# Optimization experiments

Hardware: AMD Instinct MI355X
Metric: run time of the kernel (lower is better)

## Reference

```python
import jax, jax.numpy as jnp
import numpy as np

DIM = 768


def setup_inputs() -> dict:
    key = jax.random.key(0)
    k1, k2, k3, k4, k5 = jax.random.split(key, 5)
    lines = jax.random.normal(k1, (32, 512, DIM), dtype=jnp.float32)
    videos = jax.random.normal(k2, (32, 128, DIM), dtype=jnp.float32)
    video_mask = jax.random.randint(k3, (32, 128), 0, 2, dtype=jnp.int32)
    # nn.Linear(dim, dim, bias=False) weights, applied as x @ W.T
    w_q = jax.random.normal(k4, (DIM, DIM), dtype=jnp.float32) * (DIM ** -0.5)
    w_k = jax.random.normal(k5, (DIM, DIM), dtype=jnp.float32) * (DIM ** -0.5)
    return {"lines": lines, "videos": videos, "video_mask": video_mask, "w_q": w_q, "w_k": w_k}


def reference(lines, videos, video_mask, w_q, w_k):
    scale = DIM ** -0.5
    q = jnp.einsum('bld,ed->ble', lines, w_q)   # (B, L, D)
    k = jnp.einsum('bvd,ed->bve', videos, w_k)  # (B, V, D)
    scores = jnp.einsum('bld,bvd->blv', q, k) * scale
    pad = (video_mask == 0)[:, None, :]          # (B, 1, V)
    scores = jnp.where(pad, jnp.float32(-1e9), scores)
    weights = jax.nn.softmax(scores, axis=-1)    # (B, L, V)
    return jnp.einsum('blv,bvd->bld', weights, videos)
```

## Files before the change

kernel.cpp:

```cpp
#include <hip/hip_runtime.h>

#define DIM 768
#define NB  32
#define LQ  512
#define NV  128

typedef unsigned short u16;
typedef unsigned int   u32;
typedef __bf16 bf16x8 __attribute__((ext_vector_type(8)));
typedef float  f32x4  __attribute__((ext_vector_type(4)));
typedef u16    u16x8  __attribute__((ext_vector_type(8)));
typedef u16    u16x4  __attribute__((ext_vector_type(4)));

typedef __attribute__((address_space(1))) const void gvoid;
typedef __attribute__((address_space(3))) void       svoid;

__device__ __forceinline__ u16 f2bf(float f) {
    u32 u = __float_as_uint(f);
    return (u16)((u + 0x7FFFu + ((u >> 16) & 1u)) >> 16);
}

__device__ __forceinline__ bf16x8 ld_frag(const u16* p) {
    return __builtin_bit_cast(bf16x8, *(const u16x8*)p);
}

__device__ __forceinline__ void gld16(const void* g, void* l) {
    __builtin_amdgcn_global_load_lds((gvoid*)g, (svoid*)l, 16, 0, 0);
}

__global__ __launch_bounds__(256) void cvt_kernel(const float* __restrict__ src,
                                                  u16* __restrict__ dst) {
    size_t i = (size_t)blockIdx.x * 256 + threadIdx.x;
    float4 a = ((const float4*)src)[i * 2];
    float4 b = ((const float4*)src)[i * 2 + 1];
    u16x8 o = { f2bf(a.x), f2bf(a.y), f2bf(a.z), f2bf(a.w),
                f2bf(b.x), f2bf(b.y), f2bf(b.z), f2bf(b.w) };
    ((u16x8*)dst)[i] = o;
}

__global__ __launch_bounds__(256) void vt_kernel(const float* __restrict__ videos,
                                                 u16* __restrict__ vt2,
                                                 u16* __restrict__ vbf) {
    const int b  = blockIdx.y;
    const int d0 = blockIdx.x * 64;
    const int t  = threadIdx.x;
    __shared__ u16 T[64][136];
    const float* src = videos + (size_t)b * NV * DIM;
#pragma unroll
    for (int p = 0; p < 8; ++p) {
        int f  = t + p * 256;
        int v  = f >> 4;
        int c4 = f & 15;
        float4 x = *(const float4*)(src + (size_t)v * DIM + d0 + c4 * 4);
        u16x4 o = { f2bf(x.x), f2bf(x.y), f2bf(x.z), f2bf(x.w) };
        T[c4 * 4 + 0][v] = o[0];
        T[c4 * 4 + 1][v] = o[1];
        T[c4 * 4 + 2][v] = o[2];
        T[c4 * 4 + 3][v] = o[3];
        *(u16x4*)(vbf + ((size_t)b * NV + v) * DIM + d0 + c4 * 4) = o;
    }
    __syncthreads();
#pragma unroll
    for (int p = 0; p < 4; ++p) {
        int f  = t + p * 256;
        int dl = f >> 4;
        int v8 = f & 15;
        int d  = d0 + dl;
        int it = d >> 7, wv = (d >> 4) & 7, lnn = d & 15;
        int ks = v8 >> 2, qd = v8 & 3;
        int lane = qd * 16 + lnn;
        size_t off = ((((size_t)b * 6 + it) * 8 + wv) * 4 + ks) * 512 + lane * 8;
        *(u16x8*)(vt2 + off) = *(const u16x8*)&T[dl][v8 * 8];
    }
}

__global__ __launch_bounds__(512) void proj_kernel(const u16* __restrict__ A0,
                                                   const u16* __restrict__ W0,
                                                   u16* __restrict__ C0,
                                                   const u16* __restrict__ A1,
                                                   const u16* __restrict__ W1,
                                                   u16* __restrict__ C1) {
    __shared__ u16 sA[128][64];
    __shared__ u16 sB[128][64];
    const int t    = threadIdx.x;
    const int w    = t >> 6;
    const int lane = t & 63;
    const int quad = lane >> 4;
    const int ln   = lane & 15;
    const int n0   = blockIdx.x * 128;

    const u16 *A, *W; u16 *C; int m0;
    if ((int)blockIdx.y < 128) { A = A0; W = W0; C = C0; m0 = blockIdx.y * 128; }
    else                       { A = A1; W = W1; C = C1; m0 = (blockIdx.y - 128) * 128; }

    const int wr = (w >> 2) * 64;
    const int wc = (w & 3) * 32;
    const int srow   = lane >> 3;
    const int schunk = (lane & 7) ^ srow;

    f32x4 acc[4][2] = {};
#pragma unroll
    for (int ks = 0; ks < 12; ++ks) {
        __syncthreads();
#pragma unroll
        for (int p = 0; p < 2; ++p) {
            int rb = w * 16 + p * 8;
            gld16(A + (size_t)(m0 + rb + srow) * DIM + ks * 64 + schunk * 8, &sA[rb][0]);
            gld16(W + (size_t)(n0 + rb + srow) * DIM + ks * 64 + schunk * 8, &sB[rb][0]);
        }
        __syncthreads();
#pragma unroll
        for (int kk = 0; kk < 2; ++kk) {
            bf16x8 af[4], bfr[2];
#pragma unroll
            for (int i = 0; i < 4; ++i)
                af[i]  = ld_frag(&sA[wr + i * 16 + ln][((kk * 4 + quad) ^ (ln & 7)) * 8]);
#pragma unroll
            for (int j = 0; j < 2; ++j)
                bfr[j] = ld_frag(&sB[wc + j * 16 + ln][((kk * 4 + quad) ^ (ln & 7)) * 8]);
#pragma unroll
            for (int i = 0; i < 4; ++i)
#pragma unroll
                for (int j = 0; j < 2; ++j)
                    acc[i][j] = __builtin_amdgcn_mfma_f32_16x16x32_bf16(af[i], bfr[j], acc[i][j], 0, 0, 0);
        }
    }
#pragma unroll
    for (int i = 0; i < 4; ++i)
#pragma unroll
        for (int j = 0; j < 2; ++j)
#pragma unroll
            for (int r = 0; r < 4; ++r)
                C[(size_t)(m0 + wr + i * 16 + quad * 4 + r) * DIM + n0 + wc + j * 16 + ln] =
                    f2bf(acc[i][j][r]);
}

__global__ __launch_bounds__(512) void attn_kernel(const u16* __restrict__ Q,
                                                   const u16* __restrict__ K,
                                                   const u16* __restrict__ Vt2,
                                                   const int* __restrict__ mask,
                                                   float* __restrict__ out) {
    const int b    = blockIdx.y;
    const int l0   = blockIdx.x * 64;
    const int t    = threadIdx.x;
    const int w    = t >> 6;
    const int lane = t & 63;
    const int quad = lane >> 4;
    const int ln   = lane & 15;

    __shared__ union {
        struct { u16 q[64][64]; u16 k[128][64]; } st;
        float s[64][132];
    } uA;
    __shared__ union {
        struct { u16 q[64][64]; u16 k[128][64]; } st;
        u16 p[64][136];
    } uB;
    __shared__ float sBias[128];

    const u16* Qb = Q + ((size_t)b * LQ + l0) * DIM;
    const u16* Kb = K + (size_t)b * NV * DIM;
    if (t < NV) sBias[t] = mask[b * NV + t] ? 0.0f : -1e9f;

    const int srow   = lane >> 3;
    const int schunk = (lane & 7) ^ srow;

    auto stage = [&](int ks, int sel) {
        u16 (*q)[64] = sel ? uB.st.q : uA.st.q;
        u16 (*k)[64] = sel ? uB.st.k : uA.st.k;
        gld16(Qb + (size_t)(w * 8 + srow) * DIM + ks * 64 + schunk * 8, &q[w * 8][0]);
        gld16(Kb + (size_t)(w * 16 + srow) * DIM + ks * 64 + schunk * 8, &k[w * 16][0]);
        gld16(Kb + (size_t)(w * 16 + 8 + srow) * DIM + ks * 64 + schunk * 8, &k[w * 16 + 8][0]);
    };

    f32x4 accS[4] = {};
    stage(0, 0);
#pragma unroll
    for (int ks = 0; ks < 12; ++ks) {
        __syncthreads();
        if (ks < 11) stage(ks + 1, (ks + 1) & 1);
        u16 (*q)[64] = (ks & 1) ? uB.st.q : uA.st.q;
        u16 (*k)[64] = (ks & 1) ? uB.st.k : uA.st.k;
#pragma unroll
        for (int kk = 0; kk < 2; ++kk) {
            bf16x8 bfr = ld_frag(&k[w * 16 + ln][((kk * 4 + quad) ^ (ln & 7)) * 8]);
#pragma unroll
            for (int i = 0; i < 4; ++i) {
                bf16x8 af = ld_frag(&q[i * 16 + ln][((kk * 4 + quad) ^ (ln & 7)) * 8]);
                accS[i] = __builtin_amdgcn_mfma_f32_16x16x32_bf16(af, bfr, accS[i], 0, 0, 0);
            }
        }
    }
    __syncthreads();
    const float scale = 0.03608439182435161f;
#pragma unroll
    for (int i = 0; i < 4; ++i)
#pragma unroll
        for (int r = 0; r < 4; ++r)
            uA.s[i * 16 + quad * 4 + r][w * 16 + ln] = accS[i][r] * scale;
    __syncthreads();

    {
        const int row = t >> 3, seg = t & 7;
        float vals[16];
        float mx = -3.0e38f;
#pragma unroll
        for (int c = 0; c < 4; ++c) {
            float4 x  = *(const float4*)&uA.s[row][seg * 16 + c * 4];
            float4 bz = *(const float4*)&sBias[seg * 16 + c * 4];
            float a0 = x.x + bz.x, a1 = x.y + bz.y, a2 = x.z + bz.z, a3 = x.w + bz.w;
            vals[c * 4 + 0] = a0; vals[c * 4 + 1] = a1;
            vals[c * 4 + 2] = a2; vals[c * 4 + 3] = a3;
            mx = fmaxf(mx, fmaxf(fmaxf(a0, a1), fmaxf(a2, a3)));
        }
        mx = fmaxf(mx, __shfl_xor(mx, 1));
        mx = fmaxf(mx, __shfl_xor(mx, 2));
        mx = fmaxf(mx, __shfl_xor(mx, 4));
        float sum = 0.0f;
#pragma unroll
        for (int c = 0; c < 16; ++c) { float e = __expf(vals[c] - mx); vals[c] = e; sum += e; }
        sum += __shfl_xor(sum, 1);
        sum += __shfl_xor(sum, 2);
        sum += __shfl_xor(sum, 4);
        const float inv = 1.0f / sum;
        __syncthreads();
#pragma unroll
        for (int h = 0; h < 2; ++h) {
            u16x8 pk;
#pragma unroll
            for (int e = 0; e < 8; ++e) pk[e] = f2bf(vals[h * 8 + e] * inv);
            *(u16x8*)&uB.p[row][seg * 16 + h * 8] = pk;
        }
    }
    __syncthreads();

    bf16x8 paf[4][4];
#pragma unroll
    for (int i = 0; i < 4; ++i)
#pragma unroll
        for (int ks = 0; ks < 4; ++ks)
            paf[i][ks] = ld_frag(&uB.p[i * 16 + ln][ks * 32 + quad * 8]);

    const u16* V2 = Vt2 + (size_t)b * 6 * 8 * 4 * 512;
    float*     Ob = out + ((size_t)b * LQ + l0) * DIM;
    for (int it = 0; it < 6; ++it) {
        f32x4 accO[4] = {};
#pragma unroll
        for (int ks = 0; ks < 4; ++ks) {
            bf16x8 bv = ld_frag(V2 + (((size_t)(it * 8 + w)) * 4 + ks) * 512 + lane * 8);
#pragma unroll
            for (int i = 0; i < 4; ++i)
                accO[i] = __builtin_amdgcn_mfma_f32_16x16x32_bf16(paf[i][ks], bv, accO[i], 0, 0, 0);
        }
#pragma unroll
        for (int i = 0; i < 4; ++i)
#pragma unroll
            for (int r = 0; r < 4; ++r)
                Ob[(size_t)(i * 16 + quad * 4 + r) * DIM + it * 128 + w * 16 + ln] = accO[i][r];
    }
}

extern "C" void kernel_launch(void* const* d_in, const int* in_sizes, int n_in,
                              void* d_out, int out_size, void* d_ws, size_t ws_size,
                              hipStream_t stream) {
    const float* lines  = (const float*)d_in[0];
    const float* videos = (const float*)d_in[1];
    const int*   mask   = (const int*)d_in[2];
    const float* w_q    = (const float*)d_in[3];
    const float* w_k    = (const float*)d_in[4];
    float*       out    = (float*)d_out;

    u16* qw  = (u16*)d_ws;
    u16* kw  = qw  + (size_t)NB * LQ * DIM;
    u16* vt2 = kw  + (size_t)NB * NV * DIM;
    u16* lbf = vt2 + (size_t)NB * DIM * NV;
    u16* vbf = lbf + (size_t)NB * LQ * DIM;
    u16* wqb = vbf + (size_t)NB * NV * DIM;
    u16* wkb = wqb + (size_t)DIM * DIM;

    cvt_kernel<<<(NB * LQ * DIM) / 2048, 256, 0, stream>>>(lines, lbf);
    cvt_kernel<<<(DIM * DIM)     / 2048, 256, 0, stream>>>(w_q,   wqb);
    cvt_kernel<<<(DIM * DIM)     / 2048, 256, 0, stream>>>(w_k,   wkb);
    vt_kernel  <<<dim3(DIM / 64, NB), 256, 0, stream>>>(videos, vt2, vbf);

    proj_kernel<<<dim3(DIM / 128, 160), 512, 0, stream>>>(lbf, wqb, qw, vbf, wkb, kw);
    attn_kernel<<<dim3(LQ / 64, NB), 512, 0, stream>>>(qw, kw, vt2, mask, out);
}
```

Baseline: 182.6 us.

## Merge conversion kernels into one launch and remap blocks for XCD locality

The three fp32-to-bf16 conversion launches and the video transpose launch are folded into a single prep kernel that dispatches on block index, cutting launch count and inter-kernel gaps. The projection and attention kernels switch to 1D grids whose block index is remapped so that consecutive blocks sent round-robin to the same XCD share rows or batches, aiming for better L2 reuse of A tiles and K/V data. The prep kernel now always reserves the transpose shared buffer even for conversion blocks, which may slightly lower occupancy for those blocks.

```diff
diff --git a/kernel.cpp b/kernel.cpp
--- a/kernel.cpp
+++ b/kernel.cpp
@@ -28,9 +28,12 @@
     __builtin_amdgcn_global_load_lds((gvoid*)g, (svoid*)l, 16, 0, 0);
 }
 
-__global__ __launch_bounds__(256) void cvt_kernel(const float* __restrict__ src,
-                                                  u16* __restrict__ dst) {
-    size_t i = (size_t)blockIdx.x * 256 + threadIdx.x;
+#define NL_BLK 6144
+#define NW_BLK 288
+
+__device__ __forceinline__ void cvt_body(const float* __restrict__ src,
+                                         u16* __restrict__ dst, int blk) {
+    size_t i = (size_t)blk * 256 + threadIdx.x;
     float4 a = ((const float4*)src)[i * 2];
     float4 b = ((const float4*)src)[i * 2 + 1];
     u16x8 o = { f2bf(a.x), f2bf(a.y), f2bf(a.z), f2bf(a.w),
@@ -38,26 +41,38 @@
     ((u16x8*)dst)[i] = o;
 }
 
-__global__ __launch_bounds__(256) void vt_kernel(const float* __restrict__ videos,
-                                                 u16* __restrict__ vt2,
-                                                 u16* __restrict__ vbf) {
-    const int b  = blockIdx.y;
-    const int d0 = blockIdx.x * 64;
+__global__ __launch_bounds__(256) void prep_kernel(const float* __restrict__ lines,
+                                                   const float* __restrict__ w_q,
+                                                   const float* __restrict__ w_k,
+                                                   const float* __restrict__ videos,
+                                                   u16* __restrict__ lbf,
+                                                   u16* __restrict__ wqb,
+                                                   u16* __restrict__ wkb,
+                                                   u16* __restrict__ vt2,
+                                                   u16* __restrict__ vbf) {
+    __shared__ u16 T[64][136];
+    const int bx = blockIdx.x;
+    if (bx < NL_BLK)                 { cvt_body(lines, lbf, bx); return; }
+    if (bx < NL_BLK + NW_BLK)        { cvt_body(w_q,   wqb, bx - NL_BLK); return; }
+    if (bx < NL_BLK + 2 * NW_BLK)    { cvt_body(w_k,   wkb, bx - NL_BLK - NW_BLK); return; }
+
+    const int v  = bx - (NL_BLK + 2 * NW_BLK);
+    const int b  = v / 12;
+    const int d0 = (v % 12) * 64;
     const int t  = threadIdx.x;
-    __shared__ u16 T[64][136];
     const float* src = videos + (size_t)b * NV * DIM;
 #pragma unroll
     for (int p = 0; p < 8; ++p) {
         int f  = t + p * 256;
-        int v  = f >> 4;
+        int vv = f >> 4;
         int c4 = f & 15;
-        float4 x = *(const float4*)(src + (size_t)v * DIM + d0 + c4 * 4);
+        float4 x = *(const float4*)(src + (size_t)vv * DIM + d0 + c4 * 4);
         u16x4 o = { f2bf(x.x), f2bf(x.y), f2bf(x.z), f2bf(x.w) };
-        T[c4 * 4 + 0][v] = o[0];
-        T[c4 * 4 + 1][v] = o[1];
-        T[c4 * 4 + 2][v] = o[2];
-        T[c4 * 4 + 3][v] = o[3];
-        *(u16x4*)(vbf + ((size_t)b * NV + v) * DIM + d0 + c4 * 4) = o;
+        T[c4 * 4 + 0][vv] = o[0];
+        T[c4 * 4 + 1][vv] = o[1];
+        T[c4 * 4 + 2][vv] = o[2];
+        T[c4 * 4 + 3][vv] = o[3];
+        *(u16x4*)(vbf + ((size_t)b * NV + vv) * DIM + d0 + c4 * 4) = o;
     }
     __syncthreads();
 #pragma unroll
@@ -87,11 +102,16 @@
     const int lane = t & 63;
     const int quad = lane >> 4;
     const int ln   = lane & 15;
-    const int n0   = blockIdx.x * 128;
-
-    const u16 *A, *W; u16 *C; int m0;
-    if ((int)blockIdx.y < 128) { A = A0; W = W0; C = C0; m0 = blockIdx.y * 128; }
-    else                       { A = A1; W = W1; C = C1; m0 = (blockIdx.y - 128) * 128; }
+
+    const u16 *A, *W; u16 *C; int m0, n0;
+    {
+        int i = blockIdx.x;
+        if (i < 768) { A = A0; W = W0; C = C0; }
+        else         { A = A1; W = W1; C = C1; i -= 768; }
+        int xcd = i & 7, s = i >> 3;
+        m0 = ((s / 6) * 8 + xcd) * 128;
+        n0 = (s % 6) * 128;
+    }
 
     const int wr = (w >> 2) * 64;
     const int wc = (w & 3) * 32;
@@ -140,8 +160,13 @@
                                                    const u16* __restrict__ Vt2,
                                                    const int* __restrict__ mask,
                                                    float* __restrict__ out) {
-    const int b    = blockIdx.y;
-    const int l0   = blockIdx.x * 64;
+    int b, l0;
+    {
+        int i = blockIdx.x;
+        int xcd = i & 7, s = i >> 3;
+        b  = (s >> 3) * 8 + xcd;
+        l0 = (s & 7) * 64;
+    }
     const int t    = threadIdx.x;
     const int w    = t >> 6;
     const int lane = t & 63;
@@ -278,11 +303,8 @@
     u16* wqb = vbf + (size_t)NB * NV * DIM;
     u16* wkb = wqb + (size_t)DIM * DIM;
 
-    cvt_kernel<<<(NB * LQ * DIM) / 2048, 256, 0, stream>>>(lines, lbf);
-    cvt_kernel<<<(DIM * DIM)     / 2048, 256, 0, stream>>>(w_q,   wqb);
-    cvt_kernel<<<(DIM * DIM)     / 2048, 256, 0, stream>>>(w_k,   wkb);
-    vt_kernel  <<<dim3(DIM / 64, NB), 256, 0, stream>>>(videos, vt2, vbf);
-
-    proj_kernel<<<dim3(DIM / 128, 160), 512, 0, stream>>>(lbf, wqb, qw, vbf, wkb, kw);
-    attn_kernel<<<dim3(LQ / 64, NB), 512, 0, stream>>>(qw, kw, vt2, mask, out);
-}
+    prep_kernel<<<NL_BLK + 2 * NW_BLK + 384, 256, 0, stream>>>(
+        lines, w_q, w_k, videos, lbf, wqb, wkb, vt2, vbf);
+    proj_kernel<<<960, 512, 0, stream>>>(lbf, wqb, qw, vbf, wkb, kw);
+    attn_kernel<<<256, 512, 0, stream>>>(qw, kw, vt2, mask, out);
+}
```

After: 168.5 us. 1.08x faster.
